# Kernel optimization log

Hardware: AMD Instinct MI355X
Metric: run time of the kernel (lower is better)

Reference implementation:

```python
import jax, jax.numpy as jnp
import numpy as np

B, N, D = 8, 8192, 512
HID_ATT = D // 8          # input_dim // num_heads = 64
TOPK = max(1, int(N * 0.3))  # 2457


def _mlp2(x, W1, b1, W2, b2):
    # 2-layer MLP: Linear -> GELU -> Linear (inference mode: dropout/norm off)
    h = jax.nn.gelu(x @ W1 + b1)
    return h @ W2 + b2


def setup_inputs() -> dict:
    key = jax.random.key(0)
    ks = jax.random.split(key, 9)
    s = lambda k, sh, fan: jax.random.normal(k, sh, jnp.float32) * (1.0 / np.sqrt(fan))
    return {
        "x": jax.random.normal(ks[0], (B, N, D), jnp.float32),
        # attention-score MLP: D -> HID_ATT -> 1
        "aW1": s(ks[1], (D, HID_ATT), D),
        "ab1": jnp.zeros((HID_ATT,), jnp.float32),
        "aW2": s(ks[2], (HID_ATT, 1), HID_ATT),
        "ab2": jnp.zeros((1,), jnp.float32),
        # projection MLP: D -> D -> D
        "pW1": s(ks[3], (D, D), D),
        "pb1": jnp.zeros((D,), jnp.float32),
        "pW2": s(ks[4], (D, D), D),
        "pb2": jnp.zeros((D,), jnp.float32),
    }


def reference(x, aW1, ab1, aW2, ab2, pW1, pb1, pW2, pb2):
    # per-instance attention score -> sigmoid weight, [B, N]
    weights = jax.nn.sigmoid(_mlp2(x, aW1, ab1, aW2, ab2)[..., 0])
    # top-k per bag (largest)
    topk_scores, topk_idx = jax.lax.top_k(weights, TOPK)  # [B, TOPK]
    # gather selected instances, scale by score, mean over selected -> [B, D]
    sel = jnp.take_along_axis(x, topk_idx[..., None], axis=1)  # [B, TOPK, D]
    emb = jnp.mean(sel * topk_scores[..., None], axis=1)       # [B, D]
    projection = _mlp2(emb, pW1, pb1, pW2, pb2)                # [B, D]
    return projection, weights
```

## Files before the change

### kernel.cpp

```cpp
#include <hip/hip_runtime.h>
#include <math.h>

#define B_BAGS 8
#define N_INST 8192
#define D_DIM  512
#define H_ATT  64
#define TOPK_K 2457
#define ROWS_TOTAL (B_BAGS * N_INST)

typedef __attribute__((ext_vector_type(8))) short bf16x8;
typedef __attribute__((ext_vector_type(4))) float f32x4;

#define WS_W1P_HI 0
#define WS_W1P_LO 65536
#define WS_META   131072
#define WS_PART3  131584
#define WS_PART1  (WS_PART3 + 8*64*512*4)
#define WS_PART2  (WS_PART1 + 8*8*512*4)

__device__ __forceinline__ unsigned short bf16_rn(float f) {
  unsigned int x = __float_as_uint(f);
  unsigned int r = (x + 0x7FFFu + ((x >> 16) & 1u)) >> 16;
  return (unsigned short)r;
}
__device__ __forceinline__ float bf16_f(unsigned short u) {
  return __uint_as_float(((unsigned int)u) << 16);
}
__device__ __forceinline__ float gelu_f(float v) {
  float u = 0.7978845608028654f * (v + 0.044715f * v * v * v);
  return 0.5f * v * (1.0f + tanhf(u));
}

__device__ __forceinline__ void cvt_hilo(const float4 u, const float4 v,
                                         bf16x8& h, bf16x8& l) {
  float f[8] = {u.x, u.y, u.z, u.w, v.x, v.y, v.z, v.w};
#pragma unroll
  for (int i = 0; i < 8; i++) {
    unsigned int b = __float_as_uint(f[i]);
    unsigned int hb = b & 0xFFFF0000u;
    float r = f[i] - __uint_as_float(hb);
    h[i] = (short)(b >> 16);
    l[i] = (short)(__float_as_uint(r) >> 16);
  }
}

__global__ __launch_bounds__(256) void k_prep(const float* __restrict__ aW1,
                                              unsigned short* __restrict__ hi,
                                              unsigned short* __restrict__ lo) {
  int tau = blockIdx.x * 256 + threadIdx.x;
  if (tau >= 4096) return;
  int ks = tau >> 8, t = (tau >> 6) & 3, lane = tau & 63;
  int n = t * 16 + (lane & 15);
  int kb = ks * 32 + (lane >> 4) * 8;
#pragma unroll
  for (int j = 0; j < 8; j++) {
    float v = aW1[(kb + j) * H_ATT + n];
    unsigned short h = bf16_rn(v);
    unsigned short l = bf16_rn(v - bf16_f(h));
    hi[tau * 8 + j] = h;
    lo[tau * 8 + j] = l;
  }
}

#define BM 64

__global__ __launch_bounds__(256) void k_scores(
    const float* __restrict__ x,
    const unsigned short* __restrict__ w1p_hi,
    const unsigned short* __restrict__ w1p_lo,
    const float* __restrict__ ab1, const float* __restrict__ aW2,
    const float* __restrict__ ab2, float* __restrict__ wout) {
  int tid = threadIdx.x;
  int wave = tid >> 6, lane = tid & 63;
  int c0 = lane & 15, quad = lane >> 4;
  int rowBase = blockIdx.x * BM + wave * 16;
  const int kq = quad * 8;

  const float* xr = x + (size_t)(rowBase + c0) * D_DIM;
  const unsigned short* bph = w1p_hi + lane * 8;
  const unsigned short* bpl = w1p_lo + lane * 8;

  f32x4 acc[4];
#pragma unroll
  for (int t = 0; t < 4; t++) acc[t] = (f32x4){0.f, 0.f, 0.f, 0.f};

  float4 a0, a1, na0, na1;
  bf16x8 bfh[4], bfl[4], nbh[4], nbl[4];

  a0 = *reinterpret_cast<const float4*>(xr + kq);
  a1 = *reinterpret_cast<const float4*>(xr + kq + 4);
#pragma unroll
  for (int t = 0; t < 4; t++) {
    bfh[t] = *reinterpret_cast<const bf16x8*>(bph + t * 512);
    bfl[t] = *reinterpret_cast<const bf16x8*>(bpl + t * 512);
  }

  for (int ks = 0; ks < 16; ks++) {
    if (ks < 15) {
      int kb = (ks + 1) * 32;
      na0 = *reinterpret_cast<const float4*>(xr + kb + kq);
      na1 = *reinterpret_cast<const float4*>(xr + kb + kq + 4);
      int fo = (ks + 1) * 4 * 512;
#pragma unroll
      for (int t = 0; t < 4; t++) {
        nbh[t] = *reinterpret_cast<const bf16x8*>(bph + fo + t * 512);
        nbl[t] = *reinterpret_cast<const bf16x8*>(bpl + fo + t * 512);
      }
    }
    bf16x8 afh, afl;
    cvt_hilo(a0, a1, afh, afl);
#pragma unroll
    for (int t = 0; t < 4; t++) {
      acc[t] = __builtin_amdgcn_mfma_f32_16x16x32_bf16(afl, bfh[t], acc[t], 0, 0, 0);
      acc[t] = __builtin_amdgcn_mfma_f32_16x16x32_bf16(afh, bfl[t], acc[t], 0, 0, 0);
      acc[t] = __builtin_amdgcn_mfma_f32_16x16x32_bf16(afh, bfh[t], acc[t], 0, 0, 0);
    }
    a0 = na0; a1 = na1;
#pragma unroll
    for (int t = 0; t < 4; t++) { bfh[t] = nbh[t]; bfl[t] = nbl[t]; }
  }

  float w2v[4], b1v[4];
#pragma unroll
  for (int t = 0; t < 4; t++) {
    w2v[t] = aW2[t * 16 + c0];
    b1v[t] = ab1[t * 16 + c0];
  }
  float bias2 = ab2[0];
  float p[4] = {0.f, 0.f, 0.f, 0.f};
#pragma unroll
  for (int t = 0; t < 4; t++)
#pragma unroll
    for (int r = 0; r < 4; r++) {
      float h = gelu_f(acc[t][r] + b1v[t]);
      p[r] += h * w2v[t];
    }
#pragma unroll
  for (int off = 1; off < 16; off <<= 1)
#pragma unroll
    for (int r = 0; r < 4; r++) p[r] += __shfl_xor(p[r], off, 64);
  if (c0 == 0) {
    int row = rowBase + quad * 4;
#pragma unroll
    for (int r = 0; r < 4; r++) {
      float sc = p[r] + bias2;
      wout[row + r] = 1.0f / (1.0f + expf(-sc));
    }
  }
}

__global__ __launch_bounds__(256) void k_topk(const float* __restrict__ wout,
                                              unsigned int* __restrict__ meta) {
  int b = blockIdx.x;
  const float* w = wout + b * N_INST;
  int tid = threadIdx.x;
  unsigned int v[32];
#pragma unroll
  for (int j = 0; j < 32; j++) v[j] = __float_as_uint(w[j * 256 + tid]);

  __shared__ int red[2][4];
  int lane = tid & 63, wv = tid >> 6;
  int pb = 0;

  auto blocksum = [&](int c) -> int {
#pragma unroll
    for (int off = 32; off > 0; off >>= 1) c += __shfl_down(c, off, 64);
    if (lane == 0) red[pb][wv] = c;
    __syncthreads();
    int s = red[pb][0] + red[pb][1] + red[pb][2] + red[pb][3];
    pb ^= 1;
    return s;
  };

  unsigned int lo = 0u, hi = 0x3F800001u;
  while (hi - lo > 1u) {
    unsigned int mid = lo + ((hi - lo) >> 1);
    int c = 0;
#pragma unroll
    for (int j = 0; j < 32; j++) c += (v[j] >= mid) ? 1 : 0;
    int s = blocksum(c);
    if (s >= TOPK_K) lo = mid; else hi = mid;
  }
  unsigned int T = lo;

  int c1;
  {
    int c = 0;
#pragma unroll
    for (int j = 0; j < 32; j++) c += (v[j] > T) ? 1 : 0;
    c1 = blocksum(c);
  }
  int needed = TOPK_K - c1;

  unsigned int tm = 0;
#pragma unroll
  for (int j = 0; j < 32; j++) tm |= (v[j] == T ? 1u : 0u) << j;
  int lom = -1, him = N_INST - 1;
  while (him - lom > 1) {
    int mid = (lom + him) >> 1;
    unsigned int mask = 0u;
    if (mid >= tid) {
      unsigned int jmax = (unsigned int)(mid - tid) >> 8;
      mask = (2u << jmax) - 1u;
    }
    int s = blocksum((int)__popc(tm & mask));
    if (s >= needed) him = mid; else lom = mid;
  }
  if (tid == 0) {
    meta[b] = T;
    ((int*)meta)[8 + b] = him;
  }
}

__global__ __launch_bounds__(256) void k_gather(const float* __restrict__ x,
                                                const float* __restrict__ wout,
                                                const unsigned int* __restrict__ meta,
                                                float* __restrict__ part3) {
  int b = blockIdx.x >> 6;
  int blk = blockIdx.x & 63;
  unsigned int T = meta[b];
  int Icut = ((const int*)meta)[8 + b];
  int tid = threadIdx.x;

  __shared__ int idxs[128];
  __shared__ float wgts[128];
  __shared__ int wcnt[2];
  __shared__ float4 xfer[128];

  int r = blk * 128 + tid;
  bool sel = false;
  float wvv = 0.f;
  int pos = 0;
  if (tid < 128) {
    wvv = wout[b * N_INST + r];
    unsigned int wu = __float_as_uint(wvv);
    sel = (wu > T) || (wu == T && r <= Icut);
    unsigned long long m = __ballot(sel);
    int lane = tid & 63;
    pos = __popcll(m & ((1ull << lane) - 1ull));
    if (lane == 0) wcnt[tid >> 6] = __popcll(m);
  }
  __syncthreads();
  int total = wcnt[0] + wcnt[1];
  if (sel) {
    int base = (tid >= 64) ? wcnt[0] : 0;
    idxs[base + pos] = r;
    wgts[base + pos] = wvv;
  }
  __syncthreads();

  int half = tid >> 7;
  int L = tid & 127;
  float4 acc = {0.f, 0.f, 0.f, 0.f};
  const float* xb = x + (size_t)b * N_INST * D_DIM;
  int i2 = total & ~1;
#pragma unroll 4
  for (int i = 0; i < i2; i += 2) {
    int rr = idxs[i + half];
    float ww = wgts[i + half];
    const float4 xv = *reinterpret_cast<const float4*>(xb + (size_t)rr * D_DIM + L * 4);
    acc.x += ww * xv.x; acc.y += ww * xv.y; acc.z += ww * xv.z; acc.w += ww * xv.w;
  }
  if ((total & 1) && half == 0) {
    int rr = idxs[i2];
    float ww = wgts[i2];
    const float4 xv = *reinterpret_cast<const float4*>(xb + (size_t)rr * D_DIM + L * 4);
    acc.x += ww * xv.x; acc.y += ww * xv.y; acc.z += ww * xv.z; acc.w += ww * xv.w;
  }
  if (half == 1) xfer[L] = acc;
  __syncthreads();
  if (half == 0) {
    float4 o = xfer[L];
    acc.x += o.x; acc.y += o.y; acc.z += o.z; acc.w += o.w;
    *reinterpret_cast<float4*>(part3 + (size_t)(b * 64 + blk) * D_DIM + L * 4) = acc;
  }
}

__global__ __launch_bounds__(256) void k_proj1(const float* __restrict__ part3,
                                               const float* __restrict__ pW1,
                                               float* __restrict__ part1) {
  int jt = blockIdx.x & 7, kt = blockIdx.x >> 3;
  __shared__ float emb_s[512];
  int tid = threadIdx.x;
#pragma unroll
  for (int h = 0; h < 2; h++) {
    int vi = tid + h * 256;
    int b = vi >> 6, d0 = vi & 63;
    const float* p = part3 + (size_t)b * 64 * 512 + kt * 64 + d0;
    float e = 0.f;
#pragma unroll 8
    for (int j = 0; j < 64; j++) e += p[j * 512];
    emb_s[vi] = e * (1.0f / TOPK_K);
  }
  __syncthreads();
  int col = tid & 63, bg = tid >> 6;
  float a0 = 0.f, a1 = 0.f;
  const float* wrow = pW1 + (size_t)(kt * 64) * 512 + jt * 64 + col;
#pragma unroll 8
  for (int q = 0; q < 64; q++) {
    float wq = wrow[q * 512];
    a0 += emb_s[(bg * 2) * 64 + q] * wq;
    a1 += emb_s[(bg * 2 + 1) * 64 + q] * wq;
  }
  part1[kt * 4096 + (bg * 2) * 512 + jt * 64 + col] = a0;
  part1[kt * 4096 + (bg * 2 + 1) * 512 + jt * 64 + col] = a1;
}

__global__ __launch_bounds__(256) void k_proj2(const float* __restrict__ part1,
                                               const float* __restrict__ pb1,
                                               const float* __restrict__ pW2,
                                               float* __restrict__ part2) {
  int jt = blockIdx.x & 7, kt = blockIdx.x >> 3;
  __shared__ float h_s[512];
  int tid = threadIdx.x;
#pragma unroll
  for (int h = 0; h < 2; h++) {
    int vi = tid + h * 256;
    int b = vi >> 6, j0 = vi & 63;
    int jj = kt * 64 + j0;
    float s = pb1[jj];
#pragma unroll
    for (int p = 0; p < 8; p++) s += part1[p * 4096 + b * 512 + jj];
    h_s[vi] = gelu_f(s);
  }
  __syncthreads();
  int col = tid & 63, bg = tid >> 6;
  float a0 = 0.f, a1 = 0.f;
  const float* wrow = pW2 + (size_t)(kt * 64) * 512 + jt * 64 + col;
#pragma unroll 8
  for (int q = 0; q < 64; q++) {
    float wq = wrow[q * 512];
    a0 += h_s[(bg * 2) * 64 + q] * wq;
    a1 += h_s[(bg * 2 + 1) * 64 + q] * wq;
  }
  part2[kt * 4096 + (bg * 2) * 512 + jt * 64 + col] = a0;
  part2[kt * 4096 + (bg * 2 + 1) * 512 + jt * 64 + col] = a1;
}

__global__ __launch_bounds__(512) void k_proj3(const float* __restrict__ part2,
                                               const float* __restrict__ pb2,
                                               float* __restrict__ out) {
  int o = blockIdx.x * 512 + threadIdx.x;
  int bj = o & 511;
  float s = pb2[bj];
#pragma unroll
  for (int p = 0; p < 8; p++) s += part2[p * 4096 + o];
  out[o] = s;
}

extern "C" void kernel_launch(void* const* d_in, const int* in_sizes, int n_in,
                              void* d_out, int out_size, void* d_ws, size_t ws_size,
                              hipStream_t stream) {
  (void)in_sizes; (void)n_in; (void)out_size; (void)ws_size;
  const float* x   = (const float*)d_in[0];
  const float* aW1 = (const float*)d_in[1];
  const float* ab1 = (const float*)d_in[2];
  const float* aW2 = (const float*)d_in[3];
  const float* ab2 = (const float*)d_in[4];
  const float* pW1 = (const float*)d_in[5];
  const float* pb1 = (const float*)d_in[6];
  const float* pW2 = (const float*)d_in[7];
  const float* pb2 = (const float*)d_in[8];

  float* out  = (float*)d_out;
  float* wout = out + B_BAGS * D_DIM;

  char* ws = (char*)d_ws;
  unsigned short* w1p_hi = (unsigned short*)(ws + WS_W1P_HI);
  unsigned short* w1p_lo = (unsigned short*)(ws + WS_W1P_LO);
  unsigned int*   meta   = (unsigned int*)(ws + WS_META);
  float* part3 = (float*)(ws + WS_PART3);
  float* part1 = (float*)(ws + WS_PART1);
  float* part2 = (float*)(ws + WS_PART2);

  k_prep<<<dim3(16), dim3(256), 0, stream>>>(aW1, w1p_hi, w1p_lo);
  k_scores<<<dim3(ROWS_TOTAL / BM), dim3(256), 0, stream>>>(x, w1p_hi, w1p_lo, ab1, aW2, ab2, wout);
  k_topk<<<dim3(B_BAGS), dim3(256), 0, stream>>>(wout, meta);
  k_gather<<<dim3(B_BAGS * 64), dim3(256), 0, stream>>>(x, wout, meta, part3);
  k_proj1<<<dim3(64), dim3(256), 0, stream>>>(part3, pW1, part1);
  k_proj2<<<dim3(64), dim3(256), 0, stream>>>(part1, pb1, pW2, part2);
  k_proj3<<<dim3(B_BAGS), dim3(512), 0, stream>>>(part2, pb2, out);
}
```

Baseline: 271.8 us.

## Fuse top-k into gather, double rows per scores wave, atomically reduce projection

The scores kernel now processes 32 rows per wave (BM 128), so each loaded bf16 hi/lo weight fragment is reused across two MFMA row tiles, halving weight traffic per row. The top-k threshold search is folded into the gather kernel: every one of the 512 gather blocks redundantly recomputes the bag threshold and cut index instead of reading them from a separate launch. The final projection reduction kernel is removed: proj1 seeds the output with the bias and proj2 accumulates its partials with atomicAdd. This trades two launches for redundant top-k work in 64 blocks per bag, higher register pressure in scores, and nondeterministic float summation order.

```diff
diff --git a/kernel.cpp b/kernel.cpp
--- a/kernel.cpp
+++ b/kernel.cpp
@@ -13,10 +13,8 @@
 
 #define WS_W1P_HI 0
 #define WS_W1P_LO 65536
-#define WS_META   131072
 #define WS_PART3  131584
 #define WS_PART1  (WS_PART3 + 8*64*512*4)
-#define WS_PART2  (WS_PART1 + 8*8*512*4)
 
 __device__ __forceinline__ unsigned short bf16_rn(float f) {
   unsigned int x = __float_as_uint(f);
@@ -62,7 +60,7 @@
   }
 }
 
-#define BM 64
+#define BM 128
 
 __global__ __launch_bounds__(256) void k_scores(
     const float* __restrict__ x,
@@ -73,22 +71,29 @@
   int tid = threadIdx.x;
   int wave = tid >> 6, lane = tid & 63;
   int c0 = lane & 15, quad = lane >> 4;
-  int rowBase = blockIdx.x * BM + wave * 16;
+  int rowBase = blockIdx.x * BM + wave * 32;
   const int kq = quad * 8;
 
-  const float* xr = x + (size_t)(rowBase + c0) * D_DIM;
+  const float* xr[2];
+  xr[0] = x + (size_t)(rowBase + c0) * D_DIM;
+  xr[1] = xr[0] + 16 * D_DIM;
   const unsigned short* bph = w1p_hi + lane * 8;
   const unsigned short* bpl = w1p_lo + lane * 8;
 
-  f32x4 acc[4];
-#pragma unroll
-  for (int t = 0; t < 4; t++) acc[t] = (f32x4){0.f, 0.f, 0.f, 0.f};
-
-  float4 a0, a1, na0, na1;
+  f32x4 acc[2][4];
+#pragma unroll
+  for (int s = 0; s < 2; s++)
+#pragma unroll
+    for (int t = 0; t < 4; t++) acc[s][t] = (f32x4){0.f, 0.f, 0.f, 0.f};
+
+  float4 a0[2], a1[2], na0[2], na1[2];
   bf16x8 bfh[4], bfl[4], nbh[4], nbl[4];
 
-  a0 = *reinterpret_cast<const float4*>(xr + kq);
-  a1 = *reinterpret_cast<const float4*>(xr + kq + 4);
+#pragma unroll
+  for (int s = 0; s < 2; s++) {
+    a0[s] = *reinterpret_cast<const float4*>(xr[s] + kq);
+    a1[s] = *reinterpret_cast<const float4*>(xr[s] + kq + 4);
+  }
 #pragma unroll
   for (int t = 0; t < 4; t++) {
     bfh[t] = *reinterpret_cast<const bf16x8*>(bph + t * 512);
@@ -98,8 +103,11 @@
   for (int ks = 0; ks < 16; ks++) {
     if (ks < 15) {
       int kb = (ks + 1) * 32;
-      na0 = *reinterpret_cast<const float4*>(xr + kb + kq);
-      na1 = *reinterpret_cast<const float4*>(xr + kb + kq + 4);
+#pragma unroll
+      for (int s = 0; s < 2; s++) {
+        na0[s] = *reinterpret_cast<const float4*>(xr[s] + kb + kq);
+        na1[s] = *reinterpret_cast<const float4*>(xr[s] + kb + kq + 4);
+      }
       int fo = (ks + 1) * 4 * 512;
 #pragma unroll
       for (int t = 0; t < 4; t++) {
@@ -107,15 +115,19 @@
         nbl[t] = *reinterpret_cast<const bf16x8*>(bpl + fo + t * 512);
       }
     }
-    bf16x8 afh, afl;
-    cvt_hilo(a0, a1, afh, afl);
-#pragma unroll
-    for (int t = 0; t < 4; t++) {
-      acc[t] = __builtin_amdgcn_mfma_f32_16x16x32_bf16(afl, bfh[t], acc[t], 0, 0, 0);
-      acc[t] = __builtin_amdgcn_mfma_f32_16x16x32_bf16(afh, bfl[t], acc[t], 0, 0, 0);
-      acc[t] = __builtin_amdgcn_mfma_f32_16x16x32_bf16(afh, bfh[t], acc[t], 0, 0, 0);
-    }
-    a0 = na0; a1 = na1;
+    bf16x8 afh[2], afl[2];
+#pragma unroll
+    for (int s = 0; s < 2; s++) cvt_hilo(a0[s], a1[s], afh[s], afl[s]);
+#pragma unroll
+    for (int s = 0; s < 2; s++)
+#pragma unroll
+      for (int t = 0; t < 4; t++) {
+        acc[s][t] = __builtin_amdgcn_mfma_f32_16x16x32_bf16(afl[s], bfh[t], acc[s][t], 0, 0, 0);
+        acc[s][t] = __builtin_amdgcn_mfma_f32_16x16x32_bf16(afh[s], bfl[t], acc[s][t], 0, 0, 0);
+        acc[s][t] = __builtin_amdgcn_mfma_f32_16x16x32_bf16(afh[s], bfh[t], acc[s][t], 0, 0, 0);
+      }
+#pragma unroll
+    for (int s = 0; s < 2; s++) { a0[s] = na0[s]; a1[s] = na1[s]; }
 #pragma unroll
     for (int t = 0; t < 4; t++) { bfh[t] = nbh[t]; bfl[t] = nbl[t]; }
   }
@@ -127,33 +139,39 @@
     b1v[t] = ab1[t * 16 + c0];
   }
   float bias2 = ab2[0];
-  float p[4] = {0.f, 0.f, 0.f, 0.f};
-#pragma unroll
-  for (int t = 0; t < 4; t++)
-#pragma unroll
-    for (int r = 0; r < 4; r++) {
-      float h = gelu_f(acc[t][r] + b1v[t]);
-      p[r] += h * w2v[t];
+#pragma unroll
+  for (int s = 0; s < 2; s++) {
+    float p[4] = {0.f, 0.f, 0.f, 0.f};
+#pragma unroll
+    for (int t = 0; t < 4; t++)
+#pragma unroll
+      for (int r = 0; r < 4; r++) {
+        float h = gelu_f(acc[s][t][r] + b1v[t]);
+        p[r] += h * w2v[t];
+      }
+#pragma unroll
+    for (int off = 1; off < 16; off <<= 1)
+#pragma unroll
+      for (int r = 0; r < 4; r++) p[r] += __shfl_xor(p[r], off, 64);
+    if (c0 == 0) {
+      int row = rowBase + s * 16 + quad * 4;
+#pragma unroll
+      for (int r = 0; r < 4; r++) {
+        float sc = p[r] + bias2;
+        wout[row + r] = 1.0f / (1.0f + expf(-sc));
+      }
     }
-#pragma unroll
-  for (int off = 1; off < 16; off <<= 1)
-#pragma unroll
-    for (int r = 0; r < 4; r++) p[r] += __shfl_xor(p[r], off, 64);
-  if (c0 == 0) {
-    int row = rowBase + quad * 4;
-#pragma unroll
-    for (int r = 0; r < 4; r++) {
-      float sc = p[r] + bias2;
-      wout[row + r] = 1.0f / (1.0f + expf(-sc));
-    }
-  }
-}
-
-__global__ __launch_bounds__(256) void k_topk(const float* __restrict__ wout,
-                                              unsigned int* __restrict__ meta) {
-  int b = blockIdx.x;
+  }
+}
+
+__global__ __launch_bounds__(256) void k_gather(const float* __restrict__ x,
+                                                const float* __restrict__ wout,
+                                                float* __restrict__ part3) {
+  int b = blockIdx.x >> 6;
+  int blk = blockIdx.x & 63;
+  int tid = threadIdx.x;
   const float* w = wout + b * N_INST;
-  int tid = threadIdx.x;
+
   unsigned int v[32];
 #pragma unroll
   for (int j = 0; j < 32; j++) v[j] = __float_as_uint(w[j * 256 + tid]);
@@ -161,7 +179,6 @@
   __shared__ int red[2][4];
   int lane = tid & 63, wv = tid >> 6;
   int pb = 0;
-
   auto blocksum = [&](int c) -> int {
 #pragma unroll
     for (int off = 32; off > 0; off >>= 1) c += __shfl_down(c, off, 64);
@@ -178,20 +195,14 @@
     int c = 0;
 #pragma unroll
     for (int j = 0; j < 32; j++) c += (v[j] >= mid) ? 1 : 0;
-    int s = blocksum(c);
-    if (s >= TOPK_K) lo = mid; else hi = mid;
+    if (blocksum(c) >= TOPK_K) lo = mid; else hi = mid;
   }
   unsigned int T = lo;
-
-  int c1;
-  {
-    int c = 0;
-#pragma unroll
-    for (int j = 0; j < 32; j++) c += (v[j] > T) ? 1 : 0;
-    c1 = blocksum(c);
-  }
+  int c1 = 0;
+#pragma unroll
+  for (int j = 0; j < 32; j++) c1 += (v[j] > T) ? 1 : 0;
+  c1 = blocksum(c1);
   int needed = TOPK_K - c1;
-
   unsigned int tm = 0;
 #pragma unroll
   for (int j = 0; j < 32; j++) tm |= (v[j] == T ? 1u : 0u) << j;
@@ -203,24 +214,9 @@
       unsigned int jmax = (unsigned int)(mid - tid) >> 8;
       mask = (2u << jmax) - 1u;
     }
-    int s = blocksum((int)__popc(tm & mask));
-    if (s >= needed) him = mid; else lom = mid;
-  }
-  if (tid == 0) {
-    meta[b] = T;
-    ((int*)meta)[8 + b] = him;
-  }
-}
-
-__global__ __launch_bounds__(256) void k_gather(const float* __restrict__ x,
-                                                const float* __restrict__ wout,
-                                                const unsigned int* __restrict__ meta,
-                                                float* __restrict__ part3) {
-  int b = blockIdx.x >> 6;
-  int blk = blockIdx.x & 63;
-  unsigned int T = meta[b];
-  int Icut = ((const int*)meta)[8 + b];
-  int tid = threadIdx.x;
+    if (blocksum((int)__popc(tm & mask)) >= needed) him = mid; else lom = mid;
+  }
+  int Icut = him;
 
   __shared__ int idxs[128];
   __shared__ float wgts[128];
@@ -232,11 +228,10 @@
   float wvv = 0.f;
   int pos = 0;
   if (tid < 128) {
-    wvv = wout[b * N_INST + r];
+    wvv = w[r];
     unsigned int wu = __float_as_uint(wvv);
     sel = (wu > T) || (wu == T && r <= Icut);
     unsigned long long m = __ballot(sel);
-    int lane = tid & 63;
     pos = __popcll(m & ((1ull << lane) - 1ull));
     if (lane == 0) wcnt[tid >> 6] = __popcll(m);
   }
@@ -278,10 +273,18 @@
 
 __global__ __launch_bounds__(256) void k_proj1(const float* __restrict__ part3,
                                                const float* __restrict__ pW1,
-                                               float* __restrict__ part1) {
+                                               float* __restrict__ part1,
+                                               const float* __restrict__ pb2,
+                                               float* __restrict__ out) {
   int jt = blockIdx.x & 7, kt = blockIdx.x >> 3;
   __shared__ float emb_s[512];
   int tid = threadIdx.x;
+  int col = tid & 63, bg = tid >> 6;
+  if (kt == 0) {
+    float bz = pb2[jt * 64 + col];
+    out[(bg * 2) * 512 + jt * 64 + col] = bz;
+    out[(bg * 2 + 1) * 512 + jt * 64 + col] = bz;
+  }
 #pragma unroll
   for (int h = 0; h < 2; h++) {
     int vi = tid + h * 256;
@@ -293,7 +296,6 @@
     emb_s[vi] = e * (1.0f / TOPK_K);
   }
   __syncthreads();
-  int col = tid & 63, bg = tid >> 6;
   float a0 = 0.f, a1 = 0.f;
   const float* wrow = pW1 + (size_t)(kt * 64) * 512 + jt * 64 + col;
 #pragma unroll 8
@@ -309,7 +311,7 @@
 __global__ __launch_bounds__(256) void k_proj2(const float* __restrict__ part1,
                                                const float* __restrict__ pb1,
                                                const float* __restrict__ pW2,
-                                               float* __restrict__ part2) {
+                                               float* __restrict__ out) {
   int jt = blockIdx.x & 7, kt = blockIdx.x >> 3;
   __shared__ float h_s[512];
   int tid = threadIdx.x;
@@ -333,19 +335,8 @@
     a0 += h_s[(bg * 2) * 64 + q] * wq;
     a1 += h_s[(bg * 2 + 1) * 64 + q] * wq;
   }
-  part2[kt * 4096 + (bg * 2) * 512 + jt * 64 + col] = a0;
-  part2[kt * 4096 + (bg * 2 + 1) * 512 + jt * 64 + col] = a1;
-}
-
-__global__ __launch_bounds__(512) void k_proj3(const float* __restrict__ part2,
-                                               const float* __restrict__ pb2,
-                                               float* __restrict__ out) {
-  int o = blockIdx.x * 512 + threadIdx.x;
-  int bj = o & 511;
-  float s = pb2[bj];
-#pragma unroll
-  for (int p = 0; p < 8; p++) s += part2[p * 4096 + o];
-  out[o] = s;
+  atomicAdd(&out[(bg * 2) * 512 + jt * 64 + col], a0);
+  atomicAdd(&out[(bg * 2 + 1) * 512 + jt * 64 + col], a1);
 }
 
 extern "C" void kernel_launch(void* const* d_in, const int* in_sizes, int n_in,
@@ -368,16 +359,12 @@
   char* ws = (char*)d_ws;
   unsigned short* w1p_hi = (unsigned short*)(ws + WS_W1P_HI);
   unsigned short* w1p_lo = (unsigned short*)(ws + WS_W1P_LO);
-  unsigned int*   meta   = (unsigned int*)(ws + WS_META);
   float* part3 = (float*)(ws + WS_PART3);
   float* part1 = (float*)(ws + WS_PART1);
-  float* part2 = (float*)(ws + WS_PART2);
 
   k_prep<<<dim3(16), dim3(256), 0, stream>>>(aW1, w1p_hi, w1p_lo);
   k_scores<<<dim3(ROWS_TOTAL / BM), dim3(256), 0, stream>>>(x, w1p_hi, w1p_lo, ab1, aW2, ab2, wout);
-  k_topk<<<dim3(B_BAGS), dim3(256), 0, stream>>>(wout, meta);
-  k_gather<<<dim3(B_BAGS * 64), dim3(256), 0, stream>>>(x, wout, meta, part3);
-  k_proj1<<<dim3(64), dim3(256), 0, stream>>>(part3, pW1, part1);
-  k_proj2<<<dim3(64), dim3(256), 0, stream>>>(part1, pb1, pW2, part2);
-  k_proj3<<<dim3(B_BAGS), dim3(512), 0, stream>>>(part2, pb2, out);
-}
+  k_gather<<<dim3(B_BAGS * 64), dim3(256), 0, stream>>>(x, wout, part3);
+  k_proj1<<<dim3(64), dim3(256), 0, stream>>>(part3, pW1, part1, pb2, out);
+  k_proj2<<<dim3(64), dim3(256), 0, stream>>>(part1, pb1, pW2, out);
+}
```

Measured after the change: 265.5 us. -2.3%, faster.
